# Kernel tuning notes

Hardware: AMD Instinct MI355X
Metric: run time of the kernel (lower is better)

The kernel has to match this reference:

```python
import jax, jax.numpy as jnp
import numpy as np

SIGMA = 1.0
ALPHA = 64.0
EPS = 1e-8


def setup_inputs() -> dict:
    key = jax.random.key(0)
    z = jax.random.normal(key, (8192, 1024), dtype=jnp.float32)
    return {"z": z}


def reference(z):
    # L2 normalize rows (matches F.normalize(p=2, dim=1))
    z = z / jnp.maximum(jnp.linalg.norm(z, axis=1, keepdims=True), 1e-12)
    N = z.shape[0] // 2
    z1, z2 = z[:N], z[N:]

    inv2s2 = 1.0 / (2.0 * SIGMA ** 2)

    # positive pairs: squared distance between aligned rows
    d_pos = jnp.sum((z1 - z2) ** 2, axis=1)              # [N]
    g_pos = jnp.exp(-d_pos * inv2s2)
    s_pos = jnp.log(g_pos + EPS) + 1.0                    # f' for KL

    # negative pairs: full NxN squared euclidean distance on z1
    sq = jnp.sum(z1 * z1, axis=1)                         # [N]
    d2 = sq[:, None] + sq[None, :] - 2.0 * (z1 @ z1.T)    # [N, N]
    d2 = jnp.maximum(d2, 0.0)
    g_neg = jnp.exp(-d2 * inv2s2)
    s_neg = jnp.log(g_neg + EPS) + 1.0
    star_neg = jnp.exp(s_neg - 1.0)                       # f* for KL

    # masked mean over off-diagonal entries
    offdiag = ~jnp.eye(N, dtype=bool)
    star_mean = jnp.sum(jnp.where(offdiag, star_neg, 0.0)) / (N * (N - 1))

    loss = -jnp.mean(s_pos) + ALPHA * star_mean
    return loss
```

## Files before the change

### kernel.cpp

```cpp
#include <hip/hip_runtime.h>
#include <hip/hip_bf16.h>
#include <stdint.h>


#define AS1 __attribute__((address_space(1)))
#define AS3 __attribute__((address_space(3)))

typedef unsigned short u16;
typedef uint8_t  u8;
typedef int    i32x4 __attribute__((ext_vector_type(4)));
typedef int    i32x8 __attribute__((ext_vector_type(8)));
typedef float  f32x4 __attribute__((ext_vector_type(4)));

constexpr int   D     = 1024;
constexpr int   DB    = D / 2;
constexpr int   N     = 4096;
constexpr int   TM    = 128;
constexpr int   BKB   = 128;
constexpr int   NB    = N / TM;
constexpr int   NTRI  = NB * (NB + 1) / 2;
constexpr float EPS   = 1e-8f;
constexpr float ALPHA = 64.0f;

__device__ __forceinline__ void async_load16(const void* g, void* l) {
    __builtin_amdgcn_global_load_lds((AS1 void*)g, (AS3 void*)l, 16, 0, 0);
}

__device__ __forceinline__ int fp4_of(float v) {
    const float y = fabsf(v) * 32.0f;
    int n = (y < 0.25f) ? 0 : (y < 0.75f) ? 1 : (y < 1.25f) ? 2 :
            (y < 1.75f) ? 3 : (y < 2.5f)  ? 4 : (y < 3.5f)  ? 5 :
            (y < 5.0f)  ? 6 : 7;
    return n | ((v < 0.0f) ? 8 : 0);
}

__global__ __launch_bounds__(256) void norm_spos_kernel(
    const float* __restrict__ z, u8* __restrict__ q, float* __restrict__ spos)
{
    const int row = blockIdx.x;
    const int t   = threadIdx.x;
    const int lane = t & 63, wave = t >> 6;

    const float4 a = ((const float4*)(z + (size_t)row       * D))[t];
    const float4 b = ((const float4*)(z + (size_t)(row + N) * D))[t];

    float s1 = a.x*a.x + a.y*a.y + a.z*a.z + a.w*a.w;
    float s2 = b.x*b.x + b.y*b.y + b.z*b.z + b.w*b.w;
    #pragma unroll
    for (int off = 32; off; off >>= 1) {
        s1 += __shfl_down(s1, off);
        s2 += __shfl_down(s2, off);
    }
    __shared__ float r1[4], r2[4], r3[4];
    if (lane == 0) { r1[wave] = s1; r2[wave] = s2; }
    __syncthreads();
    const float ss1 = r1[0] + r1[1] + r1[2] + r1[3];
    const float ss2 = r2[0] + r2[1] + r2[2] + r2[3];
    const float inv1 = 1.0f / fmaxf(sqrtf(ss1), 1e-12f);
    const float inv2 = 1.0f / fmaxf(sqrtf(ss2), 1e-12f);

    float4 an, bn;
    an.x = a.x * inv1; an.y = a.y * inv1; an.z = a.z * inv1; an.w = a.w * inv1;
    bn.x = b.x * inv2; bn.y = b.y * inv2; bn.z = b.z * inv2; bn.w = b.w * inv2;

    const int pk = fp4_of(an.x) | (fp4_of(an.y) << 4) |
                   (fp4_of(an.z) << 8) | (fp4_of(an.w) << 12);
    ((u16*)q)[row * (DB / 2) + t] = (u16)pk;

    const float dx = an.x - bn.x, dy = an.y - bn.y, dz = an.z - bn.z, dw = an.w - bn.w;
    float dp = dx*dx + dy*dy + dz*dz + dw*dw;
    #pragma unroll
    for (int off = 32; off; off >>= 1) dp += __shfl_down(dp, off);
    if (lane == 0) r3[wave] = dp;
    __syncthreads();
    if (t == 0) {
        const float d_pos = r3[0] + r3[1] + r3[2] + r3[3];
        const float g     = expf(-0.5f * d_pos);
        spos[row] = logf(g + EPS) + 1.0f;
    }
}

__global__ __launch_bounds__(256, 3) void gram_kernel(
    const u8* __restrict__ Q, float* __restrict__ star_part)
{
    __shared__ __align__(16) u8 lA[TM * BKB];
    __shared__ __align__(16) u8 lB[TM * BKB];
    __shared__ float wsum[4];

    int bi = 0, rem = blockIdx.x;
    while (rem >= NB - bi) { rem -= NB - bi; ++bi; }
    const int bj    = bi + rem;
    const int rowA0 = bi * TM, rowB0 = bj * TM;
    const bool diag = (bi == bj);

    const int t    = threadIdx.x;
    const int lane = t & 63;
    const int wave = t >> 6;
    const int wm   = (wave & 1) * 64;
    const int wn   = (wave >> 1) * 64;
    const int fr   = lane & 15;
    const int fq   = lane >> 4;

    const u8* gA[4]; const u8* gB[4]; u8* dA[4]; u8* dB[4];
    #pragma unroll
    for (int j = 0; j < 4; ++j) {
        const int p = t + 256 * j;
        const int r = p >> 3;
        const int c = (p & 7) ^ (r & 7);
        gA[j] = Q + (size_t)(rowA0 + r) * DB + c * 16;
        gB[j] = Q + (size_t)(rowB0 + r) * DB + c * 16;
        dA[j] = &lA[p * 16];
        dB[j] = &lB[p * 16];
    }

    f32x4 acc[4][4];
    #pragma unroll
    for (int mt = 0; mt < 4; ++mt)
        #pragma unroll
        for (int nt = 0; nt < 4; ++nt)
            acc[mt][nt] = f32x4{0.f, 0.f, 0.f, 0.f};

    for (int k0 = 0; k0 < DB; k0 += BKB) {
        #pragma unroll
        for (int j = 0; j < 4; ++j) {
            async_load16(gA[j] + k0, dA[j]);
            async_load16(gB[j] + k0, dB[j]);
        }
        __syncthreads();

        #pragma unroll
        for (int kk = 0; kk < 2; ++kk) {
            i32x8 bf[4];
            #pragma unroll
            for (int nt = 0; nt < 4; ++nt) {
                const int r = wn + nt * 16 + fr;
                const i32x4 v = ((const i32x4*)&lB[r * BKB])[(kk * 4 + fq) ^ (r & 7)];
                bf[nt][0] = v[0]; bf[nt][1] = v[1]; bf[nt][2] = v[2]; bf[nt][3] = v[3];
                bf[nt][4] = 0;    bf[nt][5] = 0;    bf[nt][6] = 0;    bf[nt][7] = 0;
            }
            #pragma unroll
            for (int mt = 0; mt < 4; ++mt) {
                const int r = wm + mt * 16 + fr;
                const i32x4 v = ((const i32x4*)&lA[r * BKB])[(kk * 4 + fq) ^ (r & 7)];
                i32x8 af;
                af[0] = v[0]; af[1] = v[1]; af[2] = v[2]; af[3] = v[3];
                af[4] = 0;    af[5] = 0;    af[6] = 0;    af[7] = 0;
                #pragma unroll
                for (int nt = 0; nt < 4; ++nt)
                    acc[mt][nt] = __builtin_amdgcn_mfma_scale_f32_16x16x128_f8f6f4(
                        af, bf[nt], acc[mt][nt],
                        4, 4,
                        0, 0x7f7f7f7f,
                        0, 0x7f7f7f7f);
            }
        }

        __syncthreads();
    }

    constexpr float INV = 1.0f / 1024.0f;
    float lsum = 0.0f;
    #pragma unroll
    for (int mt = 0; mt < 4; ++mt) {
        #pragma unroll
        for (int nt = 0; nt < 4; ++nt) {
            #pragma unroll
            for (int r = 0; r < 4; ++r) {
                const float g  = acc[mt][nt][r] * INV;
                const int   gi = wm + mt * 16 + fq * 4 + r;
                const int   gj = wn + nt * 16 + fr;
                const float d2 = fmaxf(2.0f - 2.0f * g, 0.0f);
                const float e  = __expf(-0.5f * d2);
                lsum += (diag && gi == gj) ? 0.0f : e;
            }
        }
    }
    #pragma unroll
    for (int off = 32; off; off >>= 1) lsum += __shfl_down(lsum, off);
    if (lane == 0) wsum[wave] = lsum;
    __syncthreads();
    if (t == 0)
        star_part[blockIdx.x] = (diag ? 1.0f : 2.0f) *
                                (wsum[0] + wsum[1] + wsum[2] + wsum[3]);
}

__global__ __launch_bounds__(256) void finalize_kernel(
    const float* __restrict__ spos, const float* __restrict__ star,
    float* __restrict__ out)
{
    const int t = threadIdx.x, lane = t & 63, wave = t >> 6;
    float s1 = 0.0f, s2 = 0.0f;
    for (int i = t; i < N;    i += 256) s1 += spos[i];
    for (int i = t; i < NTRI; i += 256) s2 += star[i];
    #pragma unroll
    for (int off = 32; off; off >>= 1) {
        s1 += __shfl_down(s1, off);
        s2 += __shfl_down(s2, off);
    }
    __shared__ float r1[4], r2[4];
    if (lane == 0) { r1[wave] = s1; r2[wave] = s2; }
    __syncthreads();
    if (t == 0) {
        const float spos_sum = r1[0] + r1[1] + r1[2] + r1[3];
        const float star_sum = r2[0] + r2[1] + r2[2] + r2[3];
        const float star_mean = star_sum / ((float)N * (float)(N - 1)) + EPS;
        out[0] = -spos_sum / (float)N + ALPHA * star_mean;
    }
}

extern "C" void kernel_launch(void* const* d_in, const int* in_sizes, int n_in,
                              void* d_out, int out_size, void* d_ws, size_t ws_size,
                              hipStream_t stream)
{
    (void)in_sizes; (void)n_in; (void)out_size; (void)ws_size;
    const float* z    = (const float*)d_in[0];
    float*       out  = (float*)d_out;
    u8*          q    = (u8*)d_ws;
    float*       spos = (float*)((char*)d_ws + (size_t)N * DB);
    float*       star = spos + N;

    hipLaunchKernelGGL(norm_spos_kernel, dim3(N),    dim3(256), 0, stream, z, q, spos);
    hipLaunchKernelGGL(gram_kernel,      dim3(NTRI), dim3(256), 0, stream, q, star);
    hipLaunchKernelGGL(finalize_kernel,  dim3(1),    dim3(256), 0, stream, spos, star, out);
}
```

Measured before the change: 88.42 us.

## Double-buffer gram K-loop with smaller K tile and fuse finalize via last-block atomic

The gram kernel's K step shrinks from 128 to 64 bytes, and the shared-memory tiles become double-buffered so the next tile's async global-to-LDS loads are issued before computing the current one. The separate finalize kernel is removed: the last gram block, found with an atomic counter that norm_spos_kernel resets, does the final reduction. This aims to hide load latency behind MFMA work and save one kernel launch. In exchange there are more barrier rounds per block and atomic plus fence overhead on every block.

```diff
diff --git a/kernel.cpp b/kernel.cpp
--- a/kernel.cpp
+++ b/kernel.cpp
@@ -12,15 +12,16 @@
 typedef int    i32x8 __attribute__((ext_vector_type(8)));
 typedef float  f32x4 __attribute__((ext_vector_type(4)));
 
-constexpr int   D     = 1024;
-constexpr int   DB    = D / 2;
-constexpr int   N     = 4096;
-constexpr int   TM    = 128;
-constexpr int   BKB   = 128;
-constexpr int   NB    = N / TM;
-constexpr int   NTRI  = NB * (NB + 1) / 2;
-constexpr float EPS   = 1e-8f;
-constexpr float ALPHA = 64.0f;
+constexpr int   D      = 1024;
+constexpr int   DB     = D / 2;
+constexpr int   N      = 4096;
+constexpr int   TM     = 128;
+constexpr int   BKB    = 64;
+constexpr int   ROUNDS = DB / BKB;
+constexpr int   NB     = N / TM;
+constexpr int   NTRI   = NB * (NB + 1) / 2;
+constexpr float EPS    = 1e-8f;
+constexpr float ALPHA  = 64.0f;
 
 __device__ __forceinline__ void async_load16(const void* g, void* l) {
     __builtin_amdgcn_global_load_lds((AS1 void*)g, (AS3 void*)l, 16, 0, 0);
@@ -35,12 +36,15 @@
 }
 
 __global__ __launch_bounds__(256) void norm_spos_kernel(
-    const float* __restrict__ z, u8* __restrict__ q, float* __restrict__ spos)
+    const float* __restrict__ z, u8* __restrict__ q, float* __restrict__ spos,
+    unsigned int* __restrict__ done)
 {
     const int row = blockIdx.x;
     const int t   = threadIdx.x;
     const int lane = t & 63, wave = t >> 6;
 
+    if (row == 0 && t == 0) *done = 0u;
+
     const float4 a = ((const float4*)(z + (size_t)row       * D))[t];
     const float4 b = ((const float4*)(z + (size_t)(row + N) * D))[t];
 
@@ -67,7 +71,8 @@
                    (fp4_of(an.z) << 8) | (fp4_of(an.w) << 12);
     ((u16*)q)[row * (DB / 2) + t] = (u16)pk;
 
-    const float dx = an.x - bn.x, dy = an.y - bn.y, dz = an.z - bn.z, dw = an.w - bn.w;
+    const float dx = an.x - bn.x, dy = an.y - bn.y;
+    const float dz = an.z - bn.z, dw = an.w - bn.w;
     float dp = dx*dx + dy*dy + dz*dz + dw*dw;
     #pragma unroll
     for (int off = 32; off; off >>= 1) dp += __shfl_down(dp, off);
@@ -81,11 +86,13 @@
 }
 
 __global__ __launch_bounds__(256, 3) void gram_kernel(
-    const u8* __restrict__ Q, float* __restrict__ star_part)
+    const u8* __restrict__ Q, const float* __restrict__ spos,
+    float* __restrict__ star_part, unsigned int* __restrict__ done,
+    float* __restrict__ out)
 {
-    __shared__ __align__(16) u8 lA[TM * BKB];
-    __shared__ __align__(16) u8 lB[TM * BKB];
+    __shared__ __align__(16) u8 lds[2][2][TM * BKB];
     __shared__ float wsum[4];
+    __shared__ int lastFlag;
 
     int bi = 0, rem = blockIdx.x;
     while (rem >= NB - bi) { rem -= NB - bi; ++bi; }
@@ -101,16 +108,15 @@
     const int fr   = lane & 15;
     const int fq   = lane >> 4;
 
-    const u8* gA[4]; const u8* gB[4]; u8* dA[4]; u8* dB[4];
-    #pragma unroll
-    for (int j = 0; j < 4; ++j) {
+    const u8* gAr[2]; const u8* gBr[2]; int dOff[2];
+    #pragma unroll
+    for (int j = 0; j < 2; ++j) {
         const int p = t + 256 * j;
-        const int r = p >> 3;
-        const int c = (p & 7) ^ (r & 7);
-        gA[j] = Q + (size_t)(rowA0 + r) * DB + c * 16;
-        gB[j] = Q + (size_t)(rowB0 + r) * DB + c * 16;
-        dA[j] = &lA[p * 16];
-        dB[j] = &lB[p * 16];
+        const int r = p >> 2;
+        const int c = (p & 3) ^ (r & 3);
+        gAr[j] = Q + (size_t)(rowA0 + r) * DB + c * 16;
+        gBr[j] = Q + (size_t)(rowB0 + r) * DB + c * 16;
+        dOff[j] = p * 16;
     }
 
     f32x4 acc[4][4];
@@ -120,41 +126,49 @@
         for (int nt = 0; nt < 4; ++nt)
             acc[mt][nt] = f32x4{0.f, 0.f, 0.f, 0.f};
 
-    for (int k0 = 0; k0 < DB; k0 += BKB) {
-        #pragma unroll
-        for (int j = 0; j < 4; ++j) {
-            async_load16(gA[j] + k0, dA[j]);
-            async_load16(gB[j] + k0, dB[j]);
-        }
-        __syncthreads();
-
-        #pragma unroll
-        for (int kk = 0; kk < 2; ++kk) {
-            i32x8 bf[4];
+    auto stage = [&](int rd, int buf) {
+        const int o = rd * BKB;
+        #pragma unroll
+        for (int j = 0; j < 2; ++j) {
+            async_load16(gAr[j] + o, &lds[buf][0][dOff[j]]);
+            async_load16(gBr[j] + o, &lds[buf][1][dOff[j]]);
+        }
+    };
+
+    auto compute = [&](int buf) {
+        const u8* lA = &lds[buf][0][0];
+        const u8* lB = &lds[buf][1][0];
+        i32x8 bf[4];
+        #pragma unroll
+        for (int nt = 0; nt < 4; ++nt) {
+            const int r = wn + nt * 16 + fr;
+            const i32x4 v = *(const i32x4*)(lB + r * BKB + ((fq ^ (r & 3)) * 16));
+            bf[nt][0] = v[0]; bf[nt][1] = v[1]; bf[nt][2] = v[2]; bf[nt][3] = v[3];
+            bf[nt][4] = 0;    bf[nt][5] = 0;    bf[nt][6] = 0;    bf[nt][7] = 0;
+        }
+        #pragma unroll
+        for (int mt = 0; mt < 4; ++mt) {
+            const int r = wm + mt * 16 + fr;
+            const i32x4 v = *(const i32x4*)(lA + r * BKB + ((fq ^ (r & 3)) * 16));
+            i32x8 af;
+            af[0] = v[0]; af[1] = v[1]; af[2] = v[2]; af[3] = v[3];
+            af[4] = 0;    af[5] = 0;    af[6] = 0;    af[7] = 0;
             #pragma unroll
-            for (int nt = 0; nt < 4; ++nt) {
-                const int r = wn + nt * 16 + fr;
-                const i32x4 v = ((const i32x4*)&lB[r * BKB])[(kk * 4 + fq) ^ (r & 7)];
-                bf[nt][0] = v[0]; bf[nt][1] = v[1]; bf[nt][2] = v[2]; bf[nt][3] = v[3];
-                bf[nt][4] = 0;    bf[nt][5] = 0;    bf[nt][6] = 0;    bf[nt][7] = 0;
-            }
-            #pragma unroll
-            for (int mt = 0; mt < 4; ++mt) {
-                const int r = wm + mt * 16 + fr;
-                const i32x4 v = ((const i32x4*)&lA[r * BKB])[(kk * 4 + fq) ^ (r & 7)];
-                i32x8 af;
-                af[0] = v[0]; af[1] = v[1]; af[2] = v[2]; af[3] = v[3];
-                af[4] = 0;    af[5] = 0;    af[6] = 0;    af[7] = 0;
-                #pragma unroll
-                for (int nt = 0; nt < 4; ++nt)
-                    acc[mt][nt] = __builtin_amdgcn_mfma_scale_f32_16x16x128_f8f6f4(
-                        af, bf[nt], acc[mt][nt],
-                        4, 4,
-                        0, 0x7f7f7f7f,
-                        0, 0x7f7f7f7f);
-            }
-        }
-
+            for (int nt = 0; nt < 4; ++nt)
+                acc[mt][nt] = __builtin_amdgcn_mfma_scale_f32_16x16x128_f8f6f4(
+                    af, bf[nt], acc[mt][nt],
+                    4, 4,
+                    0, 0x7f7f7f7f,
+                    0, 0x7f7f7f7f);
+        }
+    };
+
+    stage(0, 0);
+    __syncthreads();
+    for (int rd = 0; rd < ROUNDS; ++rd) {
+        const int cur = rd & 1;
+        if (rd + 1 < ROUNDS) stage(rd + 1, cur ^ 1);
+        compute(cur);
         __syncthreads();
     }
 
@@ -179,32 +193,34 @@
     for (int off = 32; off; off >>= 1) lsum += __shfl_down(lsum, off);
     if (lane == 0) wsum[wave] = lsum;
     __syncthreads();
-    if (t == 0)
+    if (t == 0) {
         star_part[blockIdx.x] = (diag ? 1.0f : 2.0f) *
                                 (wsum[0] + wsum[1] + wsum[2] + wsum[3]);
-}
-
-__global__ __launch_bounds__(256) void finalize_kernel(
-    const float* __restrict__ spos, const float* __restrict__ star,
-    float* __restrict__ out)
-{
-    const int t = threadIdx.x, lane = t & 63, wave = t >> 6;
-    float s1 = 0.0f, s2 = 0.0f;
-    for (int i = t; i < N;    i += 256) s1 += spos[i];
-    for (int i = t; i < NTRI; i += 256) s2 += star[i];
-    #pragma unroll
-    for (int off = 32; off; off >>= 1) {
-        s1 += __shfl_down(s1, off);
-        s2 += __shfl_down(s2, off);
-    }
-    __shared__ float r1[4], r2[4];
-    if (lane == 0) { r1[wave] = s1; r2[wave] = s2; }
-    __syncthreads();
-    if (t == 0) {
-        const float spos_sum = r1[0] + r1[1] + r1[2] + r1[3];
-        const float star_sum = r2[0] + r2[1] + r2[2] + r2[3];
-        const float star_mean = star_sum / ((float)N * (float)(N - 1)) + EPS;
-        out[0] = -spos_sum / (float)N + ALPHA * star_mean;
+        __threadfence();
+        const unsigned int prev = atomicAdd(done, 1u);
+        lastFlag = (prev == (unsigned int)(NTRI - 1));
+    }
+    __syncthreads();
+
+    if (lastFlag) {
+        __threadfence();
+        float s1 = 0.0f, s2 = 0.0f;
+        for (int i = t; i < N;    i += 256) s1 += spos[i];
+        for (int i = t; i < NTRI; i += 256) s2 += star_part[i];
+        #pragma unroll
+        for (int off = 32; off; off >>= 1) {
+            s1 += __shfl_down(s1, off);
+            s2 += __shfl_down(s2, off);
+        }
+        __shared__ float f1[4], f2[4];
+        if (lane == 0) { f1[wave] = s1; f2[wave] = s2; }
+        __syncthreads();
+        if (t == 0) {
+            const float spos_sum  = f1[0] + f1[1] + f1[2] + f1[3];
+            const float star_sum  = f2[0] + f2[1] + f2[2] + f2[3];
+            const float star_mean = star_sum / ((float)N * (float)(N - 1)) + EPS;
+            out[0] = -spos_sum / (float)N + ALPHA * star_mean;
+        }
     }
 }
 
@@ -213,13 +229,15 @@
                               hipStream_t stream)
 {
     (void)in_sizes; (void)n_in; (void)out_size; (void)ws_size;
-    const float* z    = (const float*)d_in[0];
-    float*       out  = (float*)d_out;
-    u8*          q    = (u8*)d_ws;
-    float*       spos = (float*)((char*)d_ws + (size_t)N * DB);
-    float*       star = spos + N;
-
-    hipLaunchKernelGGL(norm_spos_kernel, dim3(N),    dim3(256), 0, stream, z, q, spos);
-    hipLaunchKernelGGL(gram_kernel,      dim3(NTRI), dim3(256), 0, stream, q, star);
-    hipLaunchKernelGGL(finalize_kernel,  dim3(1),    dim3(256), 0, stream, spos, star, out);
-}
+    const float*  z    = (const float*)d_in[0];
+    float*        out  = (float*)d_out;
+    u8*           q    = (u8*)d_ws;
+    float*        spos = (float*)((char*)d_ws + (size_t)N * DB);
+    float*        star = spos + N;
+    unsigned int* done = (unsigned int*)(star + NTRI);
+
+    hipLaunchKernelGGL(norm_spos_kernel, dim3(N),    dim3(256), 0, stream,
+                       z, q, spos, done);
+    hipLaunchKernelGGL(gram_kernel,      dim3(NTRI), dim3(256), 0, stream,
+                       q, spos, star, done, out);
+}
```

After: 95.52 us. +8.0%, slower.
